# Kernel tuning notes

Hardware: AMD Instinct MI355X
Metric: run time of the kernel (lower is better)

Reference implementation:

```python
import jax, jax.numpy as jnp
import numpy as np

SIZE = 4096
DOWN = SIZE // 16  # reduction_factor = 16 -> 256
N_TASKS = 16
BATCH = 2048
INIT_STD = 0.01


def setup_inputs() -> dict:
    key = jax.random.key(0)
    k_x, k_t, k_wd, k_wu = jax.random.split(key, 4)
    x = jax.random.normal(k_x, (BATCH, SIZE), dtype=jnp.float32)
    task_id = jax.random.randint(k_t, (BATCH,), 0, N_TASKS)
    # Stacked per-task adapter params (init: normal(std=0.01) weights, zero bias)
    Wd = jax.random.normal(k_wd, (N_TASKS, SIZE, DOWN), dtype=jnp.float32) * INIT_STD
    bd = jnp.zeros((N_TASKS, DOWN), dtype=jnp.float32)
    Wu = jax.random.normal(k_wu, (N_TASKS, DOWN, SIZE), dtype=jnp.float32) * INIT_STD
    bu = jnp.zeros((N_TASKS, SIZE), dtype=jnp.float32)
    return {"x": x, "task_id": task_id, "Wd": Wd, "bd": bd, "Wu": Wu, "bu": bu}


def reference(x, task_id, Wd, bd, Wu, bu):
    # Down-projection for all tasks, then select each sample's routed task.
    # [B, T, DOWN] is small (B*T*256), cheaper than gathering [B, SIZE, DOWN] weights.
    down_all = jnp.einsum('bd,tdh->bth', x, Wd) + bd[None]
    down = jnp.take_along_axis(down_all, task_id[:, None, None], axis=1)[:, 0]  # [B, DOWN]
    act = jax.nn.silu(down)
    # Up-projection for all tasks, select routed task. [B, T, SIZE]
    up_all = jnp.einsum('bh,thd->btd', act, Wu) + bu[None]
    up = jnp.take_along_axis(up_all, task_id[:, None, None], axis=1)[:, 0]  # [B, SIZE]
    return x + up  # residual=True (default)
```

## Files before the change

kernel.cpp:

```cpp
#include <hip/hip_runtime.h>

#define BATCH 2048
#define SIZE 4096
#define DOWN 256
#define NTASK 16
#define KC 16
#define KCHUNK (SIZE / KC)

typedef _Float16 half8 __attribute__((ext_vector_type(8)));
typedef float floatx4 __attribute__((ext_vector_type(4)));

__device__ __forceinline__ int imin(int a, int b) { return a < b ? a : b; }

__global__ __launch_bounds__(256) void sort_kernel(const int* __restrict__ task_id,
                                                   int* __restrict__ taskOff,
                                                   int* __restrict__ sortedIdx,
                                                   int* __restrict__ taskOfPos) {
    __shared__ int cnt[NTASK];
    __shared__ int base[NTASK + 1];
    __shared__ int cur[NTASK];
    int tid = threadIdx.x;
    if (tid < NTASK) cnt[tid] = 0;
    __syncthreads();
    for (int i = tid; i < BATCH; i += 256) atomicAdd(&cnt[task_id[i]], 1);
    __syncthreads();
    if (tid == 0) {
        int s = 0;
        for (int t = 0; t < NTASK; t++) { base[t] = s; s += cnt[t]; }
        base[NTASK] = s;
    }
    __syncthreads();
    if (tid < NTASK) { cur[tid] = base[tid]; taskOff[tid] = base[tid]; }
    if (tid == 0) taskOff[NTASK] = BATCH;
    __syncthreads();
    for (int i = tid; i < BATCH; i += 256) {
        int t = task_id[i];
        int p = atomicAdd(&cur[t], 1);
        sortedIdx[p] = i;
        taskOfPos[p] = t;
    }
}

__global__ __launch_bounds__(256) void gemm1_kernel(const float* __restrict__ x,
                                                    const float* __restrict__ Wd,
                                                    const int* __restrict__ taskOff,
                                                    const int* __restrict__ sortedIdx,
                                                    _Float16* __restrict__ partial) {
    int task = blockIdx.x, kc = blockIdx.y;
    int rowStart = taskOff[task];
    int nrows = taskOff[task + 1] - rowStart;
    if (nrows <= 0) return;

    __shared__ half8 A_lds[8][65];
    __shared__ half8 B_lds[8][256];

    int tid = threadIdx.x;
    int wave = tid >> 6, lane = tid & 63, quad = lane >> 4, l15 = lane & 15;
    int kbase0 = kc * KCHUNK;
    const float* Wdt = Wd + (size_t)task * SIZE * DOWN;

    for (int r0 = 0; r0 < nrows; r0 += 64) {
        floatx4 acc[4][4];
#pragma unroll
        for (int mi = 0; mi < 4; mi++)
#pragma unroll
            for (int ni = 0; ni < 4; ni++) acc[mi][ni] = (floatx4){0.f, 0.f, 0.f, 0.f};

        int arow = tid >> 2;
        int asrc = sortedIdx[rowStart + imin(r0 + arow, nrows - 1)];
        const float* xrow = x + (size_t)asrc * SIZE;

        for (int kb = 0; kb < KCHUNK; kb += 64) {
            int kglob = kbase0 + kb;
            __syncthreads();
#pragma unroll
            for (int j = 0; j < 2; j++) {
                int kg = ((tid & 3) << 1) | j;
                const float* src = xrow + kglob + kg * 8;
                float4 f0 = *(const float4*)(src);
                float4 f1 = *(const float4*)(src + 4);
                half8 h;
                h[0] = (_Float16)f0.x; h[1] = (_Float16)f0.y;
                h[2] = (_Float16)f0.z; h[3] = (_Float16)f0.w;
                h[4] = (_Float16)f1.x; h[5] = (_Float16)f1.y;
                h[6] = (_Float16)f1.z; h[7] = (_Float16)f1.w;
                A_lds[kg][arow] = h;
            }
#pragma unroll
            for (int kg = 0; kg < 8; kg++) {
                half8 h;
#pragma unroll
                for (int i = 0; i < 8; i++)
                    h[i] = (_Float16)Wdt[(size_t)(kglob + kg * 8 + i) * DOWN + tid];
                B_lds[kg][tid] = h;
            }
            __syncthreads();
#pragma unroll
            for (int ks = 0; ks < 2; ks++) {
                int kg = ks * 4 + quad;
                half8 a[4], b[4];
#pragma unroll
                for (int i = 0; i < 4; i++) a[i] = A_lds[kg][i * 16 + l15];
#pragma unroll
                for (int i = 0; i < 4; i++) b[i] = B_lds[kg][wave * 64 + i * 16 + l15];
#pragma unroll
                for (int mi = 0; mi < 4; mi++)
#pragma unroll
                    for (int ni = 0; ni < 4; ni++)
                        acc[mi][ni] = __builtin_amdgcn_mfma_f32_16x16x32_f16(
                            a[mi], b[ni], acc[mi][ni], 0, 0, 0);
            }
        }
#pragma unroll
        for (int mi = 0; mi < 4; mi++) {
#pragma unroll
            for (int reg = 0; reg < 4; reg++) {
                int r = r0 + mi * 16 + quad * 4 + reg;
                if (r < nrows) {
                    size_t rowoff = ((size_t)kc * BATCH + (rowStart + r)) * DOWN;
#pragma unroll
                    for (int ni = 0; ni < 4; ni++) {
                        int h = wave * 64 + ni * 16 + l15;
                        partial[rowoff + h] = (_Float16)acc[mi][ni][reg];
                    }
                }
            }
        }
    }
}

__global__ __launch_bounds__(256) void silu_kernel(const _Float16* __restrict__ partial,
                                                   const float* __restrict__ bd,
                                                   const int* __restrict__ taskOfPos,
                                                   _Float16* __restrict__ act) {
    int idx = blockIdx.x * 256 + threadIdx.x;
    int s = idx >> 8, h = idx & 255;
    float v = bd[taskOfPos[s] * DOWN + h];
#pragma unroll
    for (int kc = 0; kc < KC; kc++) v += (float)partial[((size_t)kc * BATCH + s) * DOWN + h];
    float sv = v / (1.0f + __expf(-v));
    act[idx] = (_Float16)sv;
}

__global__ __launch_bounds__(256) void gemm2_kernel(const _Float16* __restrict__ act,
                                                    const float* __restrict__ Wu,
                                                    const float* __restrict__ bu,
                                                    const float* __restrict__ x,
                                                    const int* __restrict__ taskOff,
                                                    const int* __restrict__ sortedIdx,
                                                    float* __restrict__ out) {
    int task = blockIdx.x, nt = blockIdx.y;
    int rowStart = taskOff[task];
    int nrows = taskOff[task + 1] - rowStart;
    if (nrows <= 0) return;

    __shared__ half8 A_lds[8][129];
    __shared__ half8 B_lds[8][128];

    int tid = threadIdx.x;
    int wave = tid >> 6, lane = tid & 63, quad = lane >> 4, l15 = lane & 15;
    int wm = wave >> 1, wn = wave & 1;
    int ncol0 = nt * 128;
    const float* Wut = Wu + (size_t)task * DOWN * SIZE;

    for (int r0 = 0; r0 < nrows; r0 += 128) {
        floatx4 acc[4][4];
#pragma unroll
        for (int mi = 0; mi < 4; mi++)
#pragma unroll
            for (int ni = 0; ni < 4; ni++) acc[mi][ni] = (floatx4){0.f, 0.f, 0.f, 0.f};

        int arow = tid >> 1;
        int s_a = rowStart + imin(r0 + arow, nrows - 1);
        const _Float16* actrow = act + (size_t)s_a * DOWN;

        for (int kb = 0; kb < DOWN; kb += 64) {
            __syncthreads();
#pragma unroll
            for (int j = 0; j < 4; j++) {
                int kg = ((tid & 1) << 2) | j;
                A_lds[kg][arow] = *(const half8*)(actrow + kb + kg * 8);
            }
            int nl = tid & 127;
#pragma unroll
            for (int j = 0; j < 4; j++) {
                int kg = ((tid >> 7) << 2) | j;
                half8 h;
#pragma unroll
                for (int i = 0; i < 8; i++)
                    h[i] = (_Float16)Wut[(size_t)(kb + kg * 8 + i) * SIZE + ncol0 + nl];
                B_lds[kg][nl] = h;
            }
            __syncthreads();
#pragma unroll
            for (int ks = 0; ks < 2; ks++) {
                int kg = ks * 4 + quad;
                half8 a[4], b[4];
#pragma unroll
                for (int i = 0; i < 4; i++) a[i] = A_lds[kg][wm * 64 + i * 16 + l15];
#pragma unroll
                for (int i = 0; i < 4; i++) b[i] = B_lds[kg][wn * 64 + i * 16 + l15];
#pragma unroll
                for (int mi = 0; mi < 4; mi++)
#pragma unroll
                    for (int ni = 0; ni < 4; ni++)
                        acc[mi][ni] = __builtin_amdgcn_mfma_f32_16x16x32_f16(
                            a[mi], b[ni], acc[mi][ni], 0, 0, 0);
            }
        }
#pragma unroll
        for (int mi = 0; mi < 4; mi++) {
#pragma unroll
            for (int reg = 0; reg < 4; reg++) {
                int r = r0 + wm * 64 + mi * 16 + quad * 4 + reg;
                if (r < nrows) {
                    int b = sortedIdx[rowStart + r];
                    const float* xr = x + (size_t)b * SIZE;
                    float* outr = out + (size_t)b * SIZE;
#pragma unroll
                    for (int ni = 0; ni < 4; ni++) {
                        int n = ncol0 + wn * 64 + ni * 16 + l15;
                        outr[n] = acc[mi][ni][reg] + bu[task * SIZE + n] + xr[n];
                    }
                }
            }
        }
    }
}

extern "C" void kernel_launch(void* const* d_in, const int* in_sizes, int n_in,
                              void* d_out, int out_size, void* d_ws, size_t ws_size,
                              hipStream_t stream) {
    const float* x       = (const float*)d_in[0];
    const int*   task_id = (const int*)d_in[1];
    const float* Wd      = (const float*)d_in[2];
    const float* bd      = (const float*)d_in[3];
    const float* Wu      = (const float*)d_in[4];
    const float* bu      = (const float*)d_in[5];
    float* out = (float*)d_out;

    _Float16* partial = (_Float16*)d_out;
    _Float16* act     = (_Float16*)d_ws;
    int* taskOff   = (int*)(act + (size_t)BATCH * DOWN);
    int* sortedIdx = taskOff + 32;
    int* taskOfPos = sortedIdx + BATCH;

    sort_kernel<<<1, 256, 0, stream>>>(task_id, taskOff, sortedIdx, taskOfPos);
    gemm1_kernel<<<dim3(NTASK, KC), 256, 0, stream>>>(x, Wd, taskOff, sortedIdx, partial);
    silu_kernel<<<(BATCH * DOWN) / 256, 256, 0, stream>>>(partial, bd, taskOfPos, act);
    gemm2_kernel<<<dim3(NTASK, SIZE / 128), 256, 0, stream>>>(act, Wu, bu, x, taskOff,
                                                              sortedIdx, out);
}
```

Baseline: 245.6 us.

## Retile grouped GEMMs for more blocks and batch weight loads before conversion

gemm1 now splits K into 32 chunks and uses 512-thread blocks covering 128 rows, so each weight tile is reused across more rows. gemm2 uses 64-column tiles, doubling its block count. Both kernels issue all weight loads into registers before converting to fp16, to expose memory-level parallelism, and pad LDS arrays to avoid bank conflicts. The aim is to fill the GPU better with the small per-task batches. The costs are more partial-sum traffic in the split-K reduction and less reuse of A per block in gemm2.

```diff
diff --git a/kernel.cpp b/kernel.cpp
--- a/kernel.cpp
+++ b/kernel.cpp
@@ -4,7 +4,7 @@
 #define SIZE 4096
 #define DOWN 256
 #define NTASK 16
-#define KC 16
+#define KC 32
 #define KCHUNK (SIZE / KC)
 
 typedef _Float16 half8 __attribute__((ext_vector_type(8)));
@@ -41,58 +41,76 @@
     }
 }
 
-__global__ __launch_bounds__(256) void gemm1_kernel(const float* __restrict__ x,
-                                                    const float* __restrict__ Wd,
-                                                    const int* __restrict__ taskOff,
-                                                    const int* __restrict__ sortedIdx,
-                                                    _Float16* __restrict__ partial) {
+__global__ __launch_bounds__(512, 4) void gemm1_kernel(const float* __restrict__ x,
+                                                       const float* __restrict__ Wd,
+                                                       const int* __restrict__ taskOff,
+                                                       const int* __restrict__ sortedIdx,
+                                                       _Float16* __restrict__ partial) {
     int task = blockIdx.x, kc = blockIdx.y;
     int rowStart = taskOff[task];
     int nrows = taskOff[task + 1] - rowStart;
     if (nrows <= 0) return;
 
-    __shared__ half8 A_lds[8][65];
-    __shared__ half8 B_lds[8][256];
+    __shared__ half8 A_lds[8][129];
+    __shared__ half8 B_lds[8][257];
 
     int tid = threadIdx.x;
     int wave = tid >> 6, lane = tid & 63, quad = lane >> 4, l15 = lane & 15;
+    int wm = wave >> 2, wn = wave & 3;
     int kbase0 = kc * KCHUNK;
     const float* Wdt = Wd + (size_t)task * SIZE * DOWN;
 
-    for (int r0 = 0; r0 < nrows; r0 += 64) {
+    int arow = tid >> 2;
+    int kq = tid & 3;
+    int nB = tid & 255;
+    int kghB = tid >> 8;
+
+    for (int r0 = 0; r0 < nrows; r0 += 128) {
         floatx4 acc[4][4];
 #pragma unroll
         for (int mi = 0; mi < 4; mi++)
 #pragma unroll
             for (int ni = 0; ni < 4; ni++) acc[mi][ni] = (floatx4){0.f, 0.f, 0.f, 0.f};
 
-        int arow = tid >> 2;
         int asrc = sortedIdx[rowStart + imin(r0 + arow, nrows - 1)];
         const float* xrow = x + (size_t)asrc * SIZE;
 
         for (int kb = 0; kb < KCHUNK; kb += 64) {
             int kglob = kbase0 + kb;
             __syncthreads();
-#pragma unroll
-            for (int j = 0; j < 2; j++) {
-                int kg = ((tid & 3) << 1) | j;
-                const float* src = xrow + kglob + kg * 8;
+            {
+                const float* src = xrow + kglob + kq * 16;
                 float4 f0 = *(const float4*)(src);
                 float4 f1 = *(const float4*)(src + 4);
-                half8 h;
-                h[0] = (_Float16)f0.x; h[1] = (_Float16)f0.y;
-                h[2] = (_Float16)f0.z; h[3] = (_Float16)f0.w;
-                h[4] = (_Float16)f1.x; h[5] = (_Float16)f1.y;
-                h[6] = (_Float16)f1.z; h[7] = (_Float16)f1.w;
-                A_lds[kg][arow] = h;
-            }
-#pragma unroll
-            for (int kg = 0; kg < 8; kg++) {
-                half8 h;
-#pragma unroll
-                for (int i = 0; i < 8; i++)
-                    h[i] = (_Float16)Wdt[(size_t)(kglob + kg * 8 + i) * DOWN + tid];
-                B_lds[kg][tid] = h;
+                float4 f2 = *(const float4*)(src + 8);
+                float4 f3 = *(const float4*)(src + 12);
+                half8 h0, h1;
+                h0[0] = (_Float16)f0.x; h0[1] = (_Float16)f0.y;
+                h0[2] = (_Float16)f0.z; h0[3] = (_Float16)f0.w;
+                h0[4] = (_Float16)f1.x; h0[5] = (_Float16)f1.y;
+                h0[6] = (_Float16)f1.z; h0[7] = (_Float16)f1.w;
+                h1[0] = (_Float16)f2.x; h1[1] = (_Float16)f2.y;
+                h1[2] = (_Float16)f2.z; h1[3] = (_Float16)f2.w;
+                h1[4] = (_Float16)f3.x; h1[5] = (_Float16)f3.y;
+                h1[6] = (_Float16)f3.z; h1[7] = (_Float16)f3.w;
+                A_lds[kq * 2][arow] = h0;
+                A_lds[kq * 2 + 1][arow] = h1;
+            }
+            {
+                const float* Bbase = Wdt + (size_t)kglob * DOWN + nB;
+                float bv[4][8];
+#pragma unroll
+                for (int j = 0; j < 4; j++)
+#pragma unroll
+                    for (int i = 0; i < 8; i++)
+                        bv[j][i] = Bbase[(size_t)((kghB * 4 + j) * 8 + i) * DOWN];
+#pragma unroll
+                for (int j = 0; j < 4; j++) {
+                    half8 h;
+#pragma unroll
+                    for (int i = 0; i < 8; i++) h[i] = (_Float16)bv[j][i];
+                    B_lds[kghB * 4 + j][nB] = h;
+                }
             }
             __syncthreads();
 #pragma unroll
@@ -100,9 +118,9 @@
                 int kg = ks * 4 + quad;
                 half8 a[4], b[4];
 #pragma unroll
-                for (int i = 0; i < 4; i++) a[i] = A_lds[kg][i * 16 + l15];
-#pragma unroll
-                for (int i = 0; i < 4; i++) b[i] = B_lds[kg][wave * 64 + i * 16 + l15];
+                for (int i = 0; i < 4; i++) a[i] = A_lds[kg][wm * 64 + i * 16 + l15];
+#pragma unroll
+                for (int i = 0; i < 4; i++) b[i] = B_lds[kg][wn * 64 + i * 16 + l15];
 #pragma unroll
                 for (int mi = 0; mi < 4; mi++)
 #pragma unroll
@@ -115,12 +133,12 @@
         for (int mi = 0; mi < 4; mi++) {
 #pragma unroll
             for (int reg = 0; reg < 4; reg++) {
-                int r = r0 + mi * 16 + quad * 4 + reg;
+                int r = r0 + wm * 64 + mi * 16 + quad * 4 + reg;
                 if (r < nrows) {
                     size_t rowoff = ((size_t)kc * BATCH + (rowStart + r)) * DOWN;
 #pragma unroll
                     for (int ni = 0; ni < 4; ni++) {
-                        int h = wave * 64 + ni * 16 + l15;
+                        int h = wn * 64 + ni * 16 + l15;
                         partial[rowoff + h] = (_Float16)acc[mi][ni][reg];
                     }
                 }
@@ -142,35 +160,39 @@
     act[idx] = (_Float16)sv;
 }
 
-__global__ __launch_bounds__(256) void gemm2_kernel(const _Float16* __restrict__ act,
-                                                    const float* __restrict__ Wu,
-                                                    const float* __restrict__ bu,
-                                                    const float* __restrict__ x,
-                                                    const int* __restrict__ taskOff,
-                                                    const int* __restrict__ sortedIdx,
-                                                    float* __restrict__ out) {
+__global__ __launch_bounds__(256, 4) void gemm2_kernel(const _Float16* __restrict__ act,
+                                                       const float* __restrict__ Wu,
+                                                       const float* __restrict__ bu,
+                                                       const float* __restrict__ x,
+                                                       const int* __restrict__ taskOff,
+                                                       const int* __restrict__ sortedIdx,
+                                                       float* __restrict__ out) {
     int task = blockIdx.x, nt = blockIdx.y;
     int rowStart = taskOff[task];
     int nrows = taskOff[task + 1] - rowStart;
     if (nrows <= 0) return;
 
     __shared__ half8 A_lds[8][129];
-    __shared__ half8 B_lds[8][128];
+    __shared__ half8 B_lds[8][65];
 
     int tid = threadIdx.x;
     int wave = tid >> 6, lane = tid & 63, quad = lane >> 4, l15 = lane & 15;
     int wm = wave >> 1, wn = wave & 1;
-    int ncol0 = nt * 128;
+    int ncol0 = nt * 64;
     const float* Wut = Wu + (size_t)task * DOWN * SIZE;
 
+    int arow = tid >> 1;
+    int kghA = tid & 1;
+    int nB = tid & 63;
+    int kghB = tid >> 6;
+
     for (int r0 = 0; r0 < nrows; r0 += 128) {
-        floatx4 acc[4][4];
+        floatx4 acc[4][2];
 #pragma unroll
         for (int mi = 0; mi < 4; mi++)
 #pragma unroll
-            for (int ni = 0; ni < 4; ni++) acc[mi][ni] = (floatx4){0.f, 0.f, 0.f, 0.f};
-
-        int arow = tid >> 1;
+            for (int ni = 0; ni < 2; ni++) acc[mi][ni] = (floatx4){0.f, 0.f, 0.f, 0.f};
+
         int s_a = rowStart + imin(r0 + arow, nrows - 1);
         const _Float16* actrow = act + (size_t)s_a * DOWN;
 
@@ -178,32 +200,38 @@
             __syncthreads();
 #pragma unroll
             for (int j = 0; j < 4; j++) {
-                int kg = ((tid & 1) << 2) | j;
+                int kg = kghA * 4 + j;
                 A_lds[kg][arow] = *(const half8*)(actrow + kb + kg * 8);
             }
-            int nl = tid & 127;
-#pragma unroll
-            for (int j = 0; j < 4; j++) {
-                int kg = ((tid >> 7) << 2) | j;
-                half8 h;
-#pragma unroll
-                for (int i = 0; i < 8; i++)
-                    h[i] = (_Float16)Wut[(size_t)(kb + kg * 8 + i) * SIZE + ncol0 + nl];
-                B_lds[kg][nl] = h;
+            {
+                const float* Bbase = Wut + (size_t)kb * SIZE + ncol0 + nB;
+                float bv[2][8];
+#pragma unroll
+                for (int j = 0; j < 2; j++)
+#pragma unroll
+                    for (int i = 0; i < 8; i++)
+                        bv[j][i] = Bbase[(size_t)((kghB * 2 + j) * 8 + i) * SIZE];
+#pragma unroll
+                for (int j = 0; j < 2; j++) {
+                    half8 h;
+#pragma unroll
+                    for (int i = 0; i < 8; i++) h[i] = (_Float16)bv[j][i];
+                    B_lds[kghB * 2 + j][nB] = h;
+                }
             }
             __syncthreads();
 #pragma unroll
             for (int ks = 0; ks < 2; ks++) {
                 int kg = ks * 4 + quad;
-                half8 a[4], b[4];
+                half8 a[4], b[2];
 #pragma unroll
                 for (int i = 0; i < 4; i++) a[i] = A_lds[kg][wm * 64 + i * 16 + l15];
 #pragma unroll
-                for (int i = 0; i < 4; i++) b[i] = B_lds[kg][wn * 64 + i * 16 + l15];
+                for (int i = 0; i < 2; i++) b[i] = B_lds[kg][wn * 32 + i * 16 + l15];
 #pragma unroll
                 for (int mi = 0; mi < 4; mi++)
 #pragma unroll
-                    for (int ni = 0; ni < 4; ni++)
+                    for (int ni = 0; ni < 2; ni++)
                         acc[mi][ni] = __builtin_amdgcn_mfma_f32_16x16x32_f16(
                             a[mi], b[ni], acc[mi][ni], 0, 0, 0);
             }
@@ -218,8 +246,8 @@
                     const float* xr = x + (size_t)b * SIZE;
                     float* outr = out + (size_t)b * SIZE;
 #pragma unroll
-                    for (int ni = 0; ni < 4; ni++) {
-                        int n = ncol0 + wn * 64 + ni * 16 + l15;
+                    for (int ni = 0; ni < 2; ni++) {
+                        int n = ncol0 + wn * 32 + ni * 16 + l15;
                         outr[n] = acc[mi][ni][reg] + bu[task * SIZE + n] + xr[n];
                     }
                 }
@@ -246,8 +274,8 @@
     int* taskOfPos = sortedIdx + BATCH;
 
     sort_kernel<<<1, 256, 0, stream>>>(task_id, taskOff, sortedIdx, taskOfPos);
-    gemm1_kernel<<<dim3(NTASK, KC), 256, 0, stream>>>(x, Wd, taskOff, sortedIdx, partial);
+    gemm1_kernel<<<dim3(NTASK, KC), 512, 0, stream>>>(x, Wd, taskOff, sortedIdx, partial);
     silu_kernel<<<(BATCH * DOWN) / 256, 256, 0, stream>>>(partial, bd, taskOfPos, act);
-    gemm2_kernel<<<dim3(NTASK, SIZE / 128), 256, 0, stream>>>(act, Wu, bu, x, taskOff,
-                                                              sortedIdx, out);
-}
+    gemm2_kernel<<<dim3(NTASK, SIZE / 64), 256, 0, stream>>>(act, Wu, bu, x, taskOff,
+                                                             sortedIdx, out);
+}
```

Result: slower. 259.7 us (+5.7%).

## Pre-convert inputs to fp16 packed layouts and use async global-to-LDS loads

Applied to the files above, without the earlier changes.

Adds separate kernels that convert x (gathered into sorted task order) and both weight tensors into fp16, with the weights packed as k-grouped half8 vectors. The GEMMs can then load tiles with direct global-to-LDS async copies instead of strided fp32 loads with per-element conversion. gemm1 now uses a 128x128 tile split across two N blocks, and silu writes a transposed activation buffer so gemm2 can copy it contiguously. This adds extra full passes over x and the weights, plus a larger workspace, in exchange for cheaper and better coalesced GEMM loads. Weight conversion runs on every call.

```diff
diff --git a/kernel.cpp b/kernel.cpp
--- a/kernel.cpp
+++ b/kernel.cpp
@@ -1,4 +1,5 @@
 #include <hip/hip_runtime.h>
+#include <stdint.h>
 
 #define BATCH 2048
 #define SIZE 4096
@@ -6,11 +7,16 @@
 #define NTASK 16
 #define KC 16
 #define KCHUNK (SIZE / KC)
+#define XPAD 128
+#define ACTT_N (BATCH + XPAD)
 
 typedef _Float16 half8 __attribute__((ext_vector_type(8)));
 typedef float floatx4 __attribute__((ext_vector_type(4)));
 
-__device__ __forceinline__ int imin(int a, int b) { return a < b ? a : b; }
+__device__ __forceinline__ void async_cp16(void* lds, const void* g) {
+    __builtin_amdgcn_global_load_lds((const __attribute__((address_space(1))) uint32_t*)g,
+                                     (__attribute__((address_space(3))) uint32_t*)lds, 16, 0, 0);
+}
 
 __global__ __launch_bounds__(256) void sort_kernel(const int* __restrict__ task_id,
                                                    int* __restrict__ taskOff,
@@ -41,58 +47,95 @@
     }
 }
 
-__global__ __launch_bounds__(256) void gemm1_kernel(const float* __restrict__ x,
-                                                    const float* __restrict__ Wd,
-                                                    const int* __restrict__ taskOff,
+__global__ __launch_bounds__(256) void cvt_x_kernel(const float* __restrict__ x,
                                                     const int* __restrict__ sortedIdx,
-                                                    _Float16* __restrict__ partial) {
-    int task = blockIdx.x, kc = blockIdx.y;
+                                                    _Float16* __restrict__ x16) {
+    int idx = blockIdx.x * 256 + threadIdx.x;
+    int pos = idx >> 9, col = (idx & 511) * 8;
+    const float* src = x + (size_t)sortedIdx[pos] * SIZE + col;
+    float4 f0 = *(const float4*)src;
+    float4 f1 = *(const float4*)(src + 4);
+    half8 h;
+    h[0] = (_Float16)f0.x; h[1] = (_Float16)f0.y; h[2] = (_Float16)f0.z; h[3] = (_Float16)f0.w;
+    h[4] = (_Float16)f1.x; h[5] = (_Float16)f1.y; h[6] = (_Float16)f1.z; h[7] = (_Float16)f1.w;
+    *(half8*)(x16 + (size_t)pos * SIZE + col) = h;
+}
+
+__global__ __launch_bounds__(256) void cvt_w_kernel(const float* __restrict__ Wd,
+                                                    const float* __restrict__ Wu,
+                                                    half8* __restrict__ Wd16,
+                                                    half8* __restrict__ Wu16) {
+    int b = blockIdx.x, tid = threadIdx.x;
+    if (b < 8192) {
+        int idx = b * 256 + tid;
+        int n = idx & 255, kg = (idx >> 8) & 511, t = idx >> 17;
+        const float* s = Wd + ((size_t)t * SIZE + kg * 8) * DOWN + n;
+        half8 h;
+#pragma unroll
+        for (int e = 0; e < 8; e++) h[e] = (_Float16)s[(size_t)e * DOWN];
+        Wd16[idx] = h;
+    } else {
+        int idx = (b - 8192) * 256 + tid;
+        int n = idx & 4095, kg = (idx >> 12) & 31, t = idx >> 17;
+        const float* s = Wu + ((size_t)t * DOWN + kg * 8) * SIZE + n;
+        half8 h;
+#pragma unroll
+        for (int e = 0; e < 8; e++) h[e] = (_Float16)s[(size_t)e * SIZE];
+        Wu16[idx] = h;
+    }
+}
+
+__global__ __launch_bounds__(256, 4) void gemm1_kernel(const _Float16* __restrict__ x16,
+                                                       const half8* __restrict__ Wd16,
+                                                       const int* __restrict__ taskOff,
+                                                       _Float16* __restrict__ partial) {
+    int task = blockIdx.x, kc = blockIdx.y, nt = blockIdx.z;
     int rowStart = taskOff[task];
     int nrows = taskOff[task + 1] - rowStart;
     if (nrows <= 0) return;
 
-    __shared__ half8 A_lds[8][65];
-    __shared__ half8 B_lds[8][256];
+    __shared__ half8 A_lds[8][128];
+    __shared__ half8 B_lds[8][128];
 
     int tid = threadIdx.x;
     int wave = tid >> 6, lane = tid & 63, quad = lane >> 4, l15 = lane & 15;
-    int kbase0 = kc * KCHUNK;
-    const float* Wdt = Wd + (size_t)task * SIZE * DOWN;
-
-    for (int r0 = 0; r0 < nrows; r0 += 64) {
+    int wm = wave >> 1, wn = wave & 1;
+    int rowA = tid >> 1, j2 = tid & 1;
+
+    for (int r0 = 0; r0 < nrows; r0 += 128) {
         floatx4 acc[4][4];
 #pragma unroll
         for (int mi = 0; mi < 4; mi++)
 #pragma unroll
             for (int ni = 0; ni < 4; ni++) acc[mi][ni] = (floatx4){0.f, 0.f, 0.f, 0.f};
 
-        int arow = tid >> 2;
-        int asrc = sortedIdx[rowStart + imin(r0 + arow, nrows - 1)];
-        const float* xrow = x + (size_t)asrc * SIZE;
-
-        for (int kb = 0; kb < KCHUNK; kb += 64) {
-            int kglob = kbase0 + kb;
+        const _Float16* arow = x16 + (size_t)(rowStart + r0 + rowA) * SIZE;
+
+#pragma unroll
+        for (int ph = 0; ph < 4; ph++) {
+            int k0 = kc * KCHUNK + ph * 64;
             __syncthreads();
-#pragma unroll
-            for (int j = 0; j < 2; j++) {
-                int kg = ((tid & 3) << 1) | j;
-                const float* src = xrow + kglob + kg * 8;
-                float4 f0 = *(const float4*)(src);
-                float4 f1 = *(const float4*)(src + 4);
-                half8 h;
-                h[0] = (_Float16)f0.x; h[1] = (_Float16)f0.y;
-                h[2] = (_Float16)f0.z; h[3] = (_Float16)f0.w;
-                h[4] = (_Float16)f1.x; h[5] = (_Float16)f1.y;
-                h[6] = (_Float16)f1.z; h[7] = (_Float16)f1.w;
-                A_lds[kg][arow] = h;
-            }
-#pragma unroll
-            for (int kg = 0; kg < 8; kg++) {
-                half8 h;
-#pragma unroll
-                for (int i = 0; i < 8; i++)
-                    h[i] = (_Float16)Wdt[(size_t)(kglob + kg * 8 + i) * DOWN + tid];
-                B_lds[kg][tid] = h;
+            {
+                const _Float16* s = arow + k0 + j2 * 32;
+                half8 h0 = *(const half8*)(s);
+                half8 h1 = *(const half8*)(s + 8);
+                half8 h2 = *(const half8*)(s + 16);
+                half8 h3 = *(const half8*)(s + 24);
+                A_lds[j2 * 4 + 0][rowA] = h0;
+                A_lds[j2 * 4 + 1][rowA] = h1;
+                A_lds[j2 * 4 + 2][rowA] = h2;
+                A_lds[j2 * 4 + 3][rowA] = h3;
+            }
+            {
+                int kgbase = task * 512 + (k0 >> 3);
+#pragma unroll
+                for (int jj = 0; jj < 2; jj++) {
+                    int j = wave * 2 + jj;
+#pragma unroll
+                    for (int c = 0; c < 2; c++)
+                        async_cp16(&B_lds[j][c * 64],
+                                   Wd16 + (size_t)(kgbase + j) * 256 + nt * 128 + c * 64 + lane);
+                }
             }
             __syncthreads();
 #pragma unroll
@@ -100,9 +143,9 @@
                 int kg = ks * 4 + quad;
                 half8 a[4], b[4];
 #pragma unroll
-                for (int i = 0; i < 4; i++) a[i] = A_lds[kg][i * 16 + l15];
-#pragma unroll
-                for (int i = 0; i < 4; i++) b[i] = B_lds[kg][wave * 64 + i * 16 + l15];
+                for (int i = 0; i < 4; i++) a[i] = A_lds[kg][wm * 64 + i * 16 + l15];
+#pragma unroll
+                for (int i = 0; i < 4; i++) b[i] = B_lds[kg][wn * 64 + i * 16 + l15];
 #pragma unroll
                 for (int mi = 0; mi < 4; mi++)
 #pragma unroll
@@ -115,53 +158,62 @@
         for (int mi = 0; mi < 4; mi++) {
 #pragma unroll
             for (int reg = 0; reg < 4; reg++) {
-                int r = r0 + mi * 16 + quad * 4 + reg;
+                int r = r0 + wm * 64 + mi * 16 + quad * 4 + reg;
                 if (r < nrows) {
-                    size_t rowoff = ((size_t)kc * BATCH + (rowStart + r)) * DOWN;
-#pragma unroll
-                    for (int ni = 0; ni < 4; ni++) {
-                        int h = wave * 64 + ni * 16 + l15;
-                        partial[rowoff + h] = (_Float16)acc[mi][ni][reg];
-                    }
+                    size_t off = ((size_t)kc * BATCH + (rowStart + r)) * DOWN + nt * 128;
+#pragma unroll
+                    for (int ni = 0; ni < 4; ni++)
+                        partial[off + wn * 64 + ni * 16 + l15] = (_Float16)acc[mi][ni][reg];
                 }
             }
         }
     }
 }
 
-__global__ __launch_bounds__(256) void silu_kernel(const _Float16* __restrict__ partial,
+__global__ __launch_bounds__(256) void silu_kernel(const half8* __restrict__ partial8,
                                                    const float* __restrict__ bd,
                                                    const int* __restrict__ taskOfPos,
-                                                   _Float16* __restrict__ act) {
+                                                   half8* __restrict__ actT) {
     int idx = blockIdx.x * 256 + threadIdx.x;
-    int s = idx >> 8, h = idx & 255;
-    float v = bd[taskOfPos[s] * DOWN + h];
-#pragma unroll
-    for (int kc = 0; kc < KC; kc++) v += (float)partial[((size_t)kc * BATCH + s) * DOWN + h];
-    float sv = v / (1.0f + __expf(-v));
-    act[idx] = (_Float16)sv;
-}
-
-__global__ __launch_bounds__(256) void gemm2_kernel(const _Float16* __restrict__ act,
-                                                    const float* __restrict__ Wu,
-                                                    const float* __restrict__ bu,
-                                                    const float* __restrict__ x,
-                                                    const int* __restrict__ taskOff,
-                                                    const int* __restrict__ sortedIdx,
-                                                    float* __restrict__ out) {
+    int s = idx >> 5, hg = idx & 31;
+    const float* bdr = bd + taskOfPos[s] * DOWN + hg * 8;
+    float v[8];
+#pragma unroll
+    for (int e = 0; e < 8; e++) v[e] = bdr[e];
+#pragma unroll
+    for (int kc = 0; kc < KC; kc++) {
+        half8 p = partial8[((size_t)kc * BATCH + s) * 32 + hg];
+#pragma unroll
+        for (int e = 0; e < 8; e++) v[e] += (float)p[e];
+    }
+    half8 h;
+#pragma unroll
+    for (int e = 0; e < 8; e++) {
+        float sv = v[e] / (1.0f + __expf(-v[e]));
+        h[e] = (_Float16)sv;
+    }
+    actT[(size_t)hg * ACTT_N + s] = h;
+}
+
+__global__ __launch_bounds__(256, 4) void gemm2_kernel(const half8* __restrict__ actT,
+                                                       const half8* __restrict__ Wu16,
+                                                       const float* __restrict__ bu,
+                                                       const float* __restrict__ x,
+                                                       const int* __restrict__ taskOff,
+                                                       const int* __restrict__ sortedIdx,
+                                                       float* __restrict__ out) {
     int task = blockIdx.x, nt = blockIdx.y;
     int rowStart = taskOff[task];
     int nrows = taskOff[task + 1] - rowStart;
     if (nrows <= 0) return;
 
-    __shared__ half8 A_lds[8][129];
+    __shared__ half8 A_lds[8][128];
     __shared__ half8 B_lds[8][128];
 
     int tid = threadIdx.x;
     int wave = tid >> 6, lane = tid & 63, quad = lane >> 4, l15 = lane & 15;
     int wm = wave >> 1, wn = wave & 1;
     int ncol0 = nt * 128;
-    const float* Wut = Wu + (size_t)task * DOWN * SIZE;
 
     for (int r0 = 0; r0 < nrows; r0 += 128) {
         floatx4 acc[4][4];
@@ -170,26 +222,20 @@
 #pragma unroll
             for (int ni = 0; ni < 4; ni++) acc[mi][ni] = (floatx4){0.f, 0.f, 0.f, 0.f};
 
-        int arow = tid >> 1;
-        int s_a = rowStart + imin(r0 + arow, nrows - 1);
-        const _Float16* actrow = act + (size_t)s_a * DOWN;
-
-        for (int kb = 0; kb < DOWN; kb += 64) {
+#pragma unroll
+        for (int ph = 0; ph < 4; ph++) {
+            int kgbase = ph * 8;
             __syncthreads();
 #pragma unroll
-            for (int j = 0; j < 4; j++) {
-                int kg = ((tid & 1) << 2) | j;
-                A_lds[kg][arow] = *(const half8*)(actrow + kb + kg * 8);
-            }
-            int nl = tid & 127;
-#pragma unroll
-            for (int j = 0; j < 4; j++) {
-                int kg = ((tid >> 7) << 2) | j;
-                half8 h;
-#pragma unroll
-                for (int i = 0; i < 8; i++)
-                    h[i] = (_Float16)Wut[(size_t)(kb + kg * 8 + i) * SIZE + ncol0 + nl];
-                B_lds[kg][nl] = h;
+            for (int jj = 0; jj < 2; jj++) {
+                int j = wave * 2 + jj;
+#pragma unroll
+                for (int c = 0; c < 2; c++) {
+                    async_cp16(&A_lds[j][c * 64],
+                               actT + (size_t)(kgbase + j) * ACTT_N + rowStart + r0 + c * 64 + lane);
+                    async_cp16(&B_lds[j][c * 64],
+                               Wu16 + (size_t)(task * 32 + kgbase + j) * SIZE + ncol0 + c * 64 + lane);
+                }
             }
             __syncthreads();
 #pragma unroll
@@ -240,14 +286,21 @@
     float* out = (float*)d_out;
 
     _Float16* partial = (_Float16*)d_out;
-    _Float16* act     = (_Float16*)d_ws;
-    int* taskOff   = (int*)(act + (size_t)BATCH * DOWN);
+
+    char* ws = (char*)d_ws;
+    _Float16* x16 = (_Float16*)ws;            ws += (size_t)(BATCH + XPAD) * SIZE * 2;
+    half8* Wd16   = (half8*)ws;               ws += (size_t)NTASK * 512 * 256 * 16;
+    half8* Wu16   = (half8*)ws;               ws += (size_t)NTASK * 32 * 4096 * 16;
+    half8* actT   = (half8*)ws;               ws += (size_t)32 * ACTT_N * 16;
+    int* taskOff   = (int*)ws;
     int* sortedIdx = taskOff + 32;
     int* taskOfPos = sortedIdx + BATCH;
 
     sort_kernel<<<1, 256, 0, stream>>>(task_id, taskOff, sortedIdx, taskOfPos);
-    gemm1_kernel<<<dim3(NTASK, KC), 256, 0, stream>>>(x, Wd, taskOff, sortedIdx, partial);
-    silu_kernel<<<(BATCH * DOWN) / 256, 256, 0, stream>>>(partial, bd, taskOfPos, act);
-    gemm2_kernel<<<dim3(NTASK, SIZE / 128), 256, 0, stream>>>(act, Wu, bu, x, taskOff,
+    cvt_x_kernel<<<(BATCH * 512) / 256, 256, 0, stream>>>(x, sortedIdx, x16);
+    cvt_w_kernel<<<16384, 256, 0, stream>>>(Wd, Wu, Wd16, Wu16);
+    gemm1_kernel<<<dim3(NTASK, KC, 2), 256, 0, stream>>>(x16, Wd16, taskOff, partial);
+    silu_kernel<<<(BATCH * 32) / 256, 256, 0, stream>>>((const half8*)partial, bd, taskOfPos, actT);
+    gemm2_kernel<<<dim3(NTASK, SIZE / 128), 256, 0, stream>>>(actT, Wu16, bu, x, taskOff,
                                                               sortedIdx, out);
 }
```

Result: slower. 285.3 us (+16.1%).
